# Kernel tuning notes

Measured on AMD Instinct MI355X. Metric: run time of the kernel, lower is better.

The kernel has to match this reference:

```python
import jax, jax.numpy as jnp
import numpy as np

N_NODES = 100000
N_EDGES = 1600000
N_GRAPHS = 512
IN_CH = 64
HID = 64
OUT_CH = 2
NC = 3


def setup_inputs() -> dict:
    key = jax.random.key(0)
    ks = jax.random.split(key, 10)
    x = jax.random.normal(ks[0], (N_NODES, IN_CH), dtype=jnp.float32)
    edge_index = jax.random.randint(ks[1], (2, N_EDGES), 0, N_NODES, dtype=jnp.int64)
    batch = jnp.sort(jax.random.randint(ks[2], (N_NODES,), 0, N_GRAPHS, dtype=jnp.int64))
    s = 1.0 / np.sqrt(HID)
    W_rel = jax.random.normal(ks[3], (NC, HID, HID), dtype=jnp.float32) * s
    W_root = jax.random.normal(ks[4], (NC, HID, HID), dtype=jnp.float32) * s
    b_conv = jax.random.normal(ks[5], (NC, HID), dtype=jnp.float32) * s
    W1 = jax.random.normal(ks[6], (HID, 2 * HID), dtype=jnp.float32) * s
    b1 = jax.random.normal(ks[7], (2 * HID,), dtype=jnp.float32) * s
    W2 = jax.random.normal(ks[8], (2 * HID, OUT_CH), dtype=jnp.float32) * (1.0 / np.sqrt(2 * HID))
    b2 = jax.random.normal(ks[9], (OUT_CH,), dtype=jnp.float32) * (1.0 / np.sqrt(2 * HID))
    return {"x": x, "edge_index": edge_index, "batch": batch,
            "W_rel": W_rel, "W_root": W_root, "b_conv": b_conv,
            "W1": W1, "b1": b1, "W2": W2, "b2": b2}


def reference(x, edge_index, batch, W_rel, W_root, b_conv, W1, b1, W2, b2):
    src, dst = edge_index[0], edge_index[1]
    h = x
    for i in range(NC):
        # PyG GraphConv(aggr='add'): lin_rel(scatter_add(h[src] -> dst)) + lin_root(h)
        agg = jax.ops.segment_sum(h[src], dst, num_segments=N_NODES)  # [N, HID]
        h = jax.nn.relu(agg @ W_rel[i] + b_conv[i] + h @ W_root[i])
    pooled = jax.ops.segment_sum(h, batch, num_segments=N_GRAPHS)  # [G, HID]
    # MLP readout [HID, 2*HID, OUT]
    out = jax.nn.sigmoid(jax.nn.relu(pooled @ W1 + b1) @ W2 + b2)  # [G, OUT]
    return out, pooled
```

## Files before the change

### kernel.cpp

```cpp
#include <hip/hip_runtime.h>
#include <math.h>

#define N_NODES 100000
#define N_EDGES 1600000
#define N_GRAPHS 512
#define HID 64
#define NC 3

#define NBUCK 782
#define EPB 8192
#define NPBLK 196
#define PSTRIDE 3072
#define BSTRIDE 4096
#define DUMMY N_NODES
#define SRCMASK 0x1FFFF

typedef unsigned int uint;

__device__ __forceinline__ ushort f2bf(float f) {
    uint u = __float_as_uint(f);
    u += 0x7fffu + ((u >> 16) & 1u);
    return (ushort)(u >> 16);
}
__device__ __forceinline__ uint packbf2(float a, float b) {
    return (uint)f2bf(a) | ((uint)f2bf(b) << 16);
}


__global__ __launch_bounds__(512) void partition_kernel(const int* __restrict__ src,
                                                        const int* __restrict__ dst,
                                                        int* __restrict__ ccursor,
                                                        uint* __restrict__ part) {
    __shared__ int cnt[NBUCK];
    __shared__ int base[NBUCK];
    __shared__ int cur[NBUCK];
    for (int i = threadIdx.x; i < NBUCK; i += 512) { cnt[i] = 0; cur[i] = 0; }
    __syncthreads();
    const int4* d4 = (const int4*)dst;
    const int4* s4 = (const int4*)src;
    int i0 = blockIdx.x * (EPB / 4);
    int i1 = min(i0 + EPB / 4, N_EDGES / 4);
    for (int i = i0 + threadIdx.x; i < i1; i += 512) {
        int4 d = d4[i];
        atomicAdd(&cnt[d.x >> 7], 1);
        atomicAdd(&cnt[d.y >> 7], 1);
        atomicAdd(&cnt[d.z >> 7], 1);
        atomicAdd(&cnt[d.w >> 7], 1);
    }
    __syncthreads();
    for (int i = threadIdx.x; i < NBUCK; i += 512)
        base[i] = cnt[i] ? (i * PSTRIDE + atomicAdd(&ccursor[i], cnt[i])) : 0;
    __syncthreads();
    for (int i = i0 + threadIdx.x; i < i1; i += 512) {
        int4 d = d4[i];
        int4 s = s4[i];
        int b0 = d.x >> 7; part[base[b0] + atomicAdd(&cur[b0], 1)] = ((uint)(d.x & 127) << 17) | (uint)s.x;
        int b1 = d.y >> 7; part[base[b1] + atomicAdd(&cur[b1], 1)] = ((uint)(d.y & 127) << 17) | (uint)s.y;
        int b2 = d.z >> 7; part[base[b2] + atomicAdd(&cur[b2], 1)] = ((uint)(d.z & 127) << 17) | (uint)s.z;
        int b3 = d.w >> 7; part[base[b3] + atomicAdd(&cur[b3], 1)] = ((uint)(d.w & 127) << 17) | (uint)s.w;
    }
}


__global__ __launch_bounds__(256) void bcsr_kernel(const uint* __restrict__ part,
                                                   const int* __restrict__ ccursor,
                                                   int* __restrict__ row_ptr,
                                                   int* __restrict__ pdeg,
                                                   int* __restrict__ col) {
    __shared__ int deg[128];
    __shared__ int cur[128];
    __shared__ int pre[128];
    __shared__ int ss[256];
    int b = blockIdx.x;
    int t = threadIdx.x;
    int s0 = b * PSTRIDE;
    int s1 = s0 + ccursor[b];
    if (t < 128) { deg[t] = 0; cur[t] = 0; }
    __syncthreads();
    for (int e = s0 + t; e < s1; e += 256)
        atomicAdd(&deg[part[e] >> 17], 1);
    __syncthreads();
    int v = (t < 128) ? ((deg[t] + 7) & ~7) : 0;
    int val = v;
    ss[t] = val;
    __syncthreads();
    for (int off = 1; off < 256; off <<= 1) {
        int o = (t >= off) ? ss[t - off] : 0;
        __syncthreads();
        val += o;
        ss[t] = val;
        __syncthreads();
    }
    if (t < 128) pre[t] = val - v;
    __syncthreads();
    int base = b * BSTRIDE;
    int node = b * 128 + t;
    if (t < 128 && node < N_NODES) {
        row_ptr[node] = base + pre[t];
        pdeg[node] = v;
    }
    for (int e = s0 + t; e < s1; e += 256) {
        uint p = part[e];
        int nl = p >> 17;
        int r = atomicAdd(&cur[nl], 1);
        col[base + pre[nl] + r] = (int)(p & SRCMASK);
    }
    __syncthreads();
    if (t < 128) {
        for (int i = deg[t]; i < v; i++)
            col[base + pre[t] + i] = DUMMY;
    }
}


__global__ __launch_bounds__(256) void cvt_kernel(const float* __restrict__ x,
                                                  ushort* __restrict__ hX,
                                                  ushort* __restrict__ hA,
                                                  ushort* __restrict__ hB) {
    if (blockIdx.x == 0 && threadIdx.x < HID) {
        hX[(size_t)N_NODES * HID + threadIdx.x] = 0;
        hA[(size_t)N_NODES * HID + threadIdx.x] = 0;
        hB[(size_t)N_NODES * HID + threadIdx.x] = 0;
    }
    int i = blockIdx.x * blockDim.x + threadIdx.x;
    int stride = gridDim.x * blockDim.x;
    const float4* x4 = (const float4*)x;
    for (; i < N_NODES * HID / 4; i += stride) {
        float4 v = x4[i];
        uint2 o;
        o.x = packbf2(v.x, v.y);
        o.y = packbf2(v.z, v.w);
        *(uint2*)(hX + (size_t)i * 4) = o;
    }
}


__global__ __launch_bounds__(256) void wprep_kernel(const float* __restrict__ W_rel,
                                                    const float* __restrict__ W_root,
                                                    ushort* __restrict__ WT) {
    int i = blockIdx.x * blockDim.x + threadIdx.x;
    if (i >= NC * 2 * HID * HID) return;
    int l = i / (2 * HID * HID);
    int rem = i % (2 * HID * HID);
    int m = rem / (HID * HID);
    int j = rem % (HID * HID);
    int colc = j / HID;
    int k = j % HID;
    const float* W = (m ? W_root : W_rel) + l * HID * HID;
    WT[i] = f2bf(W[k * HID + colc]);
}


#define ACC4(A, v) { A.x += __uint_as_float((v).x << 16); \
                     A.y += __uint_as_float((v).x & 0xffff0000u); \
                     A.z += __uint_as_float((v).y << 16); \
                     A.w += __uint_as_float((v).y & 0xffff0000u); }

__global__ __launch_bounds__(256) void gather_kernel(
    const ushort* __restrict__ hin, ushort* __restrict__ agg,
    const int* __restrict__ row_ptr, const int* __restrict__ pdeg,
    const int* __restrict__ col)
{
    int lane = threadIdx.x & 63;
    int slot = lane >> 4;
    int ch   = (lane & 15) * 4;
    int gwid = (blockIdx.x * blockDim.x + threadIdx.x) >> 6;
    int nwaves = (gridDim.x * blockDim.x) >> 6;

    for (int n0 = gwid * 4; n0 < N_NODES; n0 += nwaves * 4) {
        int n = n0 + slot;
        const int* row = col + row_ptr[n];
        int pd = pdeg[n];
        float4 a0 = {0.f,0.f,0.f,0.f}, a1 = {0.f,0.f,0.f,0.f};
        float4 a2 = {0.f,0.f,0.f,0.f}, a3 = {0.f,0.f,0.f,0.f};
        for (int e = 0; e < pd; e += 8) {
            int4 ca = *(const int4*)(row + e);
            int4 cb = *(const int4*)(row + e + 4);
            uint2 v0 = *(const uint2*)(hin + (size_t)ca.x * HID + ch);
            uint2 v1 = *(const uint2*)(hin + (size_t)ca.y * HID + ch);
            uint2 v2 = *(const uint2*)(hin + (size_t)ca.z * HID + ch);
            uint2 v3 = *(const uint2*)(hin + (size_t)ca.w * HID + ch);
            uint2 v4 = *(const uint2*)(hin + (size_t)cb.x * HID + ch);
            uint2 v5 = *(const uint2*)(hin + (size_t)cb.y * HID + ch);
            uint2 v6 = *(const uint2*)(hin + (size_t)cb.z * HID + ch);
            uint2 v7 = *(const uint2*)(hin + (size_t)cb.w * HID + ch);
            ACC4(a0, v0); ACC4(a1, v1); ACC4(a2, v2); ACC4(a3, v3);
            ACC4(a0, v4); ACC4(a1, v5); ACC4(a2, v6); ACC4(a3, v7);
        }
        a0.x += a1.x + a2.x + a3.x;
        a0.y += a1.y + a2.y + a3.y;
        a0.z += a1.z + a2.z + a3.z;
        a0.w += a1.w + a2.w + a3.w;
        uint2 o;
        o.x = packbf2(a0.x, a0.y);
        o.y = packbf2(a0.z, a0.w);
        *(uint2*)(agg + (size_t)n * HID + ch) = o;
    }
}


__global__ __launch_bounds__(256) void transform_kernel(
    const ushort* __restrict__ hin, const ushort* __restrict__ agg,
    ushort* __restrict__ hout, const ushort* __restrict__ WTl,
    const float* __restrict__ bias)
{
    typedef __attribute__((ext_vector_type(8))) short short8;
    typedef __attribute__((ext_vector_type(4))) float f32x4;
    __shared__ float lds[4][16][68];
    int lane = threadIdx.x & 63;
    int wid  = threadIdx.x >> 6;
    int mrow = lane & 15;
    int kg   = lane >> 4;
    int gw = (blockIdx.x * blockDim.x + threadIdx.x) >> 6;
    int nw = (gridDim.x * blockDim.x) >> 6;

    short8 Bf[4][4];
#pragma unroll
    for (int c = 0; c < 4; c++)
#pragma unroll
        for (int m = 0; m < 2; m++)
#pragma unroll
            for (int h = 0; h < 2; h++)
                Bf[c][m * 2 + h] = *(const short8*)(
                    WTl + m * HID * HID + (c * 16 + mrow) * HID + h * 32 + kg * 8);

    float bv[4];
#pragma unroll
    for (int c = 0; c < 4; c++) bv[c] = bias[c * 16 + mrow];

    for (int ng = gw; ng < N_NODES / 16; ng += nw) {
        size_t rb = ((size_t)ng * 16 + mrow) * HID + kg * 8;
        short8 Ah0 = *(const short8*)(hin + rb);
        short8 Ah1 = *(const short8*)(hin + rb + 32);
        short8 Aa0 = *(const short8*)(agg + rb);
        short8 Aa1 = *(const short8*)(agg + rb + 32);
#pragma unroll
        for (int c = 0; c < 4; c++) {
            f32x4 acc = {0.f, 0.f, 0.f, 0.f};
            acc = __builtin_amdgcn_mfma_f32_16x16x32_bf16(Aa0, Bf[c][0], acc, 0, 0, 0);
            acc = __builtin_amdgcn_mfma_f32_16x16x32_bf16(Aa1, Bf[c][1], acc, 0, 0, 0);
            acc = __builtin_amdgcn_mfma_f32_16x16x32_bf16(Ah0, Bf[c][2], acc, 0, 0, 0);
            acc = __builtin_amdgcn_mfma_f32_16x16x32_bf16(Ah1, Bf[c][3], acc, 0, 0, 0);
#pragma unroll
            for (int r = 0; r < 4; r++)
                lds[wid][kg * 4 + r][c * 16 + mrow] = fmaxf(acc[r] + bv[c], 0.f);
        }
        asm volatile("s_waitcnt lgkmcnt(0)" ::: "memory");
        const float* lr = &lds[wid][mrow][kg * 16];
        float4 f0 = *(const float4*)(lr + 0);
        float4 f1 = *(const float4*)(lr + 4);
        float4 f2 = *(const float4*)(lr + 8);
        float4 f3 = *(const float4*)(lr + 12);
        uint4 o0, o1;
        o0.x = packbf2(f0.x, f0.y); o0.y = packbf2(f0.z, f0.w);
        o0.z = packbf2(f1.x, f1.y); o0.w = packbf2(f1.z, f1.w);
        o1.x = packbf2(f2.x, f2.y); o1.y = packbf2(f2.z, f2.w);
        o1.z = packbf2(f3.x, f3.y); o1.w = packbf2(f3.z, f3.w);
        ushort* orow = hout + ((size_t)ng * 16 + mrow) * HID + kg * 16;
        *(uint4*)(orow) = o0;
        *(uint4*)(orow + 8) = o1;
    }
}


__global__ __launch_bounds__(256) void pool_kernel(
    const ushort* __restrict__ h, const int* __restrict__ batch,
    float* __restrict__ pooled_ws) {
    const int CH = 64;
    int lane = threadIdx.x & 63;
    int gwid = (blockIdx.x * blockDim.x + threadIdx.x) >> 6;
    int n0 = gwid * CH;
    if (n0 >= N_NODES) return;
    int nend = min(n0 + CH, N_NODES);
    int cur = batch[n0];
    float acc = 0.f;
    for (int n = n0; n < nend; n++) {
        int g = batch[n];
        if (g != cur) {
            atomicAdd(&pooled_ws[cur * HID + lane], acc);
            acc = 0.f;
            cur = g;
        }
        acc += __uint_as_float(((uint)h[(size_t)n * HID + lane]) << 16);
    }
    atomicAdd(&pooled_ws[cur * HID + lane], acc);
}


__global__ void mlp_kernel(const float* __restrict__ pooled_ws,
                           const float* __restrict__ W1, const float* __restrict__ b1,
                           const float* __restrict__ W2, const float* __restrict__ b2,
                           float* __restrict__ out, float* __restrict__ pooled_out) {
    __shared__ float sp[HID];
    __shared__ float red[4];
    int g = blockIdx.x, t = threadIdx.x;
    if (t < HID) {
        float v = pooled_ws[g * HID + t];
        sp[t] = v;
        pooled_out[g * HID + t] = v;
    }
    __syncthreads();
    float acc = b1[t];
#pragma unroll
    for (int k = 0; k < HID; k++) acc = fmaf(sp[k], W1[k * 128 + t], acc);
    float hid = fmaxf(acc, 0.f);
    float p0 = hid * W2[t * 2 + 0];
    float p1 = hid * W2[t * 2 + 1];
    for (int off = 32; off > 0; off >>= 1) {
        p0 += __shfl_down(p0, off, 64);
        p1 += __shfl_down(p1, off, 64);
    }
    int wave = t >> 6, lane = t & 63;
    if (lane == 0) { red[wave * 2 + 0] = p0; red[wave * 2 + 1] = p1; }
    __syncthreads();
    if (t == 0) {
        float o0 = red[0] + red[2] + b2[0];
        float o1 = red[1] + red[3] + b2[1];
        out[g * 2 + 0] = 1.f / (1.f + expf(-o0));
        out[g * 2 + 1] = 1.f / (1.f + expf(-o1));
    }
}


extern "C" void kernel_launch(void* const* d_in, const int* in_sizes, int n_in,
                              void* d_out, int out_size, void* d_ws, size_t ws_size,
                              hipStream_t stream) {
    const float* x      = (const float*)d_in[0];
    const int*   ei     = (const int*)d_in[1];
    const int*   batch  = (const int*)d_in[2];
    const float* W_rel  = (const float*)d_in[3];
    const float* W_root = (const float*)d_in[4];
    const float* b_conv = (const float*)d_in[5];
    const float* W1     = (const float*)d_in[6];
    const float* b1     = (const float*)d_in[7];
    const float* W2     = (const float*)d_in[8];
    const float* b2     = (const float*)d_in[9];

    float* outp       = (float*)d_out;
    float* pooled_out = (float*)d_out + N_GRAPHS * 2;

    const size_t HROWS_B = ((size_t)(N_NODES + 1) * HID * 2 + 255) & ~(size_t)255;

    char* ws = (char*)d_ws;
    size_t off = 0;
    ushort* hX = (ushort*)(ws + off); off += HROWS_B;
    ushort* hA = (ushort*)(ws + off); off += HROWS_B;
    ushort* hB = (ushort*)(ws + off); off += HROWS_B;
    ushort* gg = (ushort*)(ws + off); off += ((size_t)N_NODES * HID * 2 + 255) & ~(size_t)255;
    ushort* WT = (ushort*)(ws + off); off += ((size_t)NC * 2 * HID * HID * 2 + 255) & ~(size_t)255;
    uint* part    = (uint*)(ws + off); off += (size_t)NBUCK * PSTRIDE * 4;
    int* colidx   = (int*)(ws + off); off += (size_t)NBUCK * BSTRIDE * 4;
    int* row_ptr  = (int*)(ws + off); off += (size_t)(N_NODES + 4) * 4;
    int* pdeg     = (int*)(ws + off); off += (size_t)(N_NODES + 4) * 4;
    int* ccursor  = (int*)(ws + off); off += (size_t)NBUCK * 4;
    float* pooled_ws = (float*)(ws + off); off += (size_t)N_GRAPHS * HID * 4;

    const int* esrc = ei;
    const int* edst = ei + N_EDGES;

    hipMemsetAsync(ccursor, 0, (size_t)NBUCK * 4, stream);
    hipMemsetAsync(pooled_ws, 0, (size_t)N_GRAPHS * HID * 4, stream);

    cvt_kernel<<<2048, 256, 0, stream>>>(x, hX, hA, hB);
    wprep_kernel<<<(NC * 2 * HID * HID + 255) / 256, 256, 0, stream>>>(W_rel, W_root, WT);

    partition_kernel<<<NPBLK, 512, 0, stream>>>(esrc, edst, ccursor, part);
    bcsr_kernel<<<NBUCK, 256, 0, stream>>>(part, ccursor, row_ptr, pdeg, colidx);

    gather_kernel<<<2048, 256, 0, stream>>>(hX, gg, row_ptr, pdeg, colidx);
    transform_kernel<<<512, 256, 0, stream>>>(hX, gg, hA, WT + 0 * 2 * HID * HID, b_conv + 0 * HID);
    gather_kernel<<<2048, 256, 0, stream>>>(hA, gg, row_ptr, pdeg, colidx);
    transform_kernel<<<512, 256, 0, stream>>>(hA, gg, hB, WT + 1 * 2 * HID * HID, b_conv + 1 * HID);
    gather_kernel<<<2048, 256, 0, stream>>>(hB, gg, row_ptr, pdeg, colidx);
    transform_kernel<<<512, 256, 0, stream>>>(hB, gg, hA, WT + 2 * 2 * HID * HID, b_conv + 2 * HID);

    pool_kernel<<<391, 256, 0, stream>>>(hA, batch, pooled_ws);
    mlp_kernel<<<N_GRAPHS, 128, 0, stream>>>(pooled_ws, W1, b1, W2, b2, outp, pooled_out);
}
```

Baseline: 290.5 us.

## Fuse gather and transform into one per-layer kernel via LDS staging

Merges the neighbour gather and the MFMA transform of each GraphConv layer into one layer_kernel. Each wave aggregates 16 nodes into LDS and feeds them straight to the bf16 MFMA, so the global agg buffer's write and re-read go away and three launches are saved. It also folds weight prep into the conversion kernel and doubles the partition block size and edges per block. The cost is a fixed one-block-per-64-nodes grid with no grid-stride loop, and padding rows/row_ptr past N_NODES so the last partial tile reads valid zeros.

```diff
diff --git a/kernel.cpp b/kernel.cpp
--- a/kernel.cpp
+++ b/kernel.cpp
@@ -8,12 +8,13 @@
 #define NC 3
 
 #define NBUCK 782
-#define EPB 8192
-#define NPBLK 196
+#define EPB 16384
+#define NPBLK 98
 #define PSTRIDE 3072
 #define BSTRIDE 4096
 #define DUMMY N_NODES
 #define SRCMASK 0x1FFFF
+#define NFBLK 1563
 
 typedef unsigned int uint;
 
@@ -27,20 +28,20 @@
 }
 
 
-__global__ __launch_bounds__(512) void partition_kernel(const int* __restrict__ src,
-                                                        const int* __restrict__ dst,
-                                                        int* __restrict__ ccursor,
-                                                        uint* __restrict__ part) {
+__global__ __launch_bounds__(1024) void partition_kernel(const int* __restrict__ src,
+                                                         const int* __restrict__ dst,
+                                                         int* __restrict__ ccursor,
+                                                         uint* __restrict__ part) {
     __shared__ int cnt[NBUCK];
     __shared__ int base[NBUCK];
     __shared__ int cur[NBUCK];
-    for (int i = threadIdx.x; i < NBUCK; i += 512) { cnt[i] = 0; cur[i] = 0; }
+    for (int i = threadIdx.x; i < NBUCK; i += 1024) { cnt[i] = 0; cur[i] = 0; }
     __syncthreads();
     const int4* d4 = (const int4*)dst;
     const int4* s4 = (const int4*)src;
     int i0 = blockIdx.x * (EPB / 4);
     int i1 = min(i0 + EPB / 4, N_EDGES / 4);
-    for (int i = i0 + threadIdx.x; i < i1; i += 512) {
+    for (int i = i0 + threadIdx.x; i < i1; i += 1024) {
         int4 d = d4[i];
         atomicAdd(&cnt[d.x >> 7], 1);
         atomicAdd(&cnt[d.y >> 7], 1);
@@ -48,10 +49,10 @@
         atomicAdd(&cnt[d.w >> 7], 1);
     }
     __syncthreads();
-    for (int i = threadIdx.x; i < NBUCK; i += 512)
+    for (int i = threadIdx.x; i < NBUCK; i += 1024)
         base[i] = cnt[i] ? (i * PSTRIDE + atomicAdd(&ccursor[i], cnt[i])) : 0;
     __syncthreads();
-    for (int i = i0 + threadIdx.x; i < i1; i += 512) {
+    for (int i = i0 + threadIdx.x; i < i1; i += 1024) {
         int4 d = d4[i];
         int4 s = s4[i];
         int b0 = d.x >> 7; part[base[b0] + atomicAdd(&cur[b0], 1)] = ((uint)(d.x & 127) << 17) | (uint)s.x;
@@ -116,38 +117,41 @@
 __global__ __launch_bounds__(256) void cvt_kernel(const float* __restrict__ x,
                                                   ushort* __restrict__ hX,
                                                   ushort* __restrict__ hA,
-                                                  ushort* __restrict__ hB) {
-    if (blockIdx.x == 0 && threadIdx.x < HID) {
-        hX[(size_t)N_NODES * HID + threadIdx.x] = 0;
-        hA[(size_t)N_NODES * HID + threadIdx.x] = 0;
-        hB[(size_t)N_NODES * HID + threadIdx.x] = 0;
-    }
-    int i = blockIdx.x * blockDim.x + threadIdx.x;
+                                                  ushort* __restrict__ hB,
+                                                  const float* __restrict__ W_rel,
+                                                  const float* __restrict__ W_root,
+                                                  ushort* __restrict__ WT,
+                                                  int* __restrict__ row_ptr,
+                                                  int* __restrict__ pdeg) {
+    int gid = blockIdx.x * blockDim.x + threadIdx.x;
     int stride = gridDim.x * blockDim.x;
+    if (gid < HID) {
+        hX[(size_t)N_NODES * HID + gid] = 0;
+        hA[(size_t)N_NODES * HID + gid] = 0;
+        hB[(size_t)N_NODES * HID + gid] = 0;
+    }
+    if (gid < 64) {
+        pdeg[N_NODES + gid] = 0;
+        row_ptr[N_NODES + gid] = 0;
+    }
     const float4* x4 = (const float4*)x;
-    for (; i < N_NODES * HID / 4; i += stride) {
+    for (int i = gid; i < N_NODES * HID / 4; i += stride) {
         float4 v = x4[i];
         uint2 o;
         o.x = packbf2(v.x, v.y);
         o.y = packbf2(v.z, v.w);
         *(uint2*)(hX + (size_t)i * 4) = o;
     }
-}
-
-
-__global__ __launch_bounds__(256) void wprep_kernel(const float* __restrict__ W_rel,
-                                                    const float* __restrict__ W_root,
-                                                    ushort* __restrict__ WT) {
-    int i = blockIdx.x * blockDim.x + threadIdx.x;
-    if (i >= NC * 2 * HID * HID) return;
-    int l = i / (2 * HID * HID);
-    int rem = i % (2 * HID * HID);
-    int m = rem / (HID * HID);
-    int j = rem % (HID * HID);
-    int colc = j / HID;
-    int k = j % HID;
-    const float* W = (m ? W_root : W_rel) + l * HID * HID;
-    WT[i] = f2bf(W[k * HID + colc]);
+    for (int i = gid; i < NC * 2 * HID * HID; i += stride) {
+        int l = i / (2 * HID * HID);
+        int rem = i % (2 * HID * HID);
+        int m = rem / (HID * HID);
+        int j = rem % (HID * HID);
+        int colc = j / HID;
+        int k = j % HID;
+        const float* W = (m ? W_root : W_rel) + l * HID * HID;
+        WT[i] = f2bf(W[k * HID + colc]);
+    }
 }
 
 
@@ -156,19 +160,25 @@
                      A.z += __uint_as_float((v).y << 16); \
                      A.w += __uint_as_float((v).y & 0xffff0000u); }
 
-__global__ __launch_bounds__(256) void gather_kernel(
-    const ushort* __restrict__ hin, ushort* __restrict__ agg,
+__global__ __launch_bounds__(256) void layer_kernel(
+    const ushort* __restrict__ hin, ushort* __restrict__ hout,
     const int* __restrict__ row_ptr, const int* __restrict__ pdeg,
-    const int* __restrict__ col)
+    const int* __restrict__ col, const ushort* __restrict__ WTl,
+    const float* __restrict__ bias)
 {
+    typedef __attribute__((ext_vector_type(8))) short short8;
+    typedef __attribute__((ext_vector_type(4))) float f32x4;
+    __shared__ ushort sagg[4][16][80];
     int lane = threadIdx.x & 63;
+    int w = threadIdx.x >> 6;
+    int nbase = blockIdx.x * 64 + w * 16;
+
     int slot = lane >> 4;
-    int ch   = (lane & 15) * 4;
-    int gwid = (blockIdx.x * blockDim.x + threadIdx.x) >> 6;
-    int nwaves = (gridDim.x * blockDim.x) >> 6;
-
-    for (int n0 = gwid * 4; n0 < N_NODES; n0 += nwaves * 4) {
-        int n = n0 + slot;
+    int ch = (lane & 15) * 4;
+#pragma unroll
+    for (int p = 0; p < 4; p++) {
+        int nl = p * 4 + slot;
+        int n = nbase + nl;
         const int* row = col + row_ptr[n];
         int pd = pdeg[n];
         float4 a0 = {0.f,0.f,0.f,0.f}, a1 = {0.f,0.f,0.f,0.f};
@@ -194,26 +204,11 @@
         uint2 o;
         o.x = packbf2(a0.x, a0.y);
         o.y = packbf2(a0.z, a0.w);
-        *(uint2*)(agg + (size_t)n * HID + ch) = o;
-    }
-}
-
-
-__global__ __launch_bounds__(256) void transform_kernel(
-    const ushort* __restrict__ hin, const ushort* __restrict__ agg,
-    ushort* __restrict__ hout, const ushort* __restrict__ WTl,
-    const float* __restrict__ bias)
-{
-    typedef __attribute__((ext_vector_type(8))) short short8;
-    typedef __attribute__((ext_vector_type(4))) float f32x4;
-    __shared__ float lds[4][16][68];
-    int lane = threadIdx.x & 63;
-    int wid  = threadIdx.x >> 6;
+        *(uint2*)&sagg[w][nl][ch] = o;
+    }
+
     int mrow = lane & 15;
-    int kg   = lane >> 4;
-    int gw = (blockIdx.x * blockDim.x + threadIdx.x) >> 6;
-    int nw = (gridDim.x * blockDim.x) >> 6;
-
+    int kg = lane >> 4;
     short8 Bf[4][4];
 #pragma unroll
     for (int c = 0; c < 4; c++)
@@ -223,40 +218,33 @@
             for (int h = 0; h < 2; h++)
                 Bf[c][m * 2 + h] = *(const short8*)(
                     WTl + m * HID * HID + (c * 16 + mrow) * HID + h * 32 + kg * 8);
-
     float bv[4];
 #pragma unroll
     for (int c = 0; c < 4; c++) bv[c] = bias[c * 16 + mrow];
 
-    for (int ng = gw; ng < N_NODES / 16; ng += nw) {
-        size_t rb = ((size_t)ng * 16 + mrow) * HID + kg * 8;
-        short8 Ah0 = *(const short8*)(hin + rb);
-        short8 Ah1 = *(const short8*)(hin + rb + 32);
-        short8 Aa0 = *(const short8*)(agg + rb);
-        short8 Aa1 = *(const short8*)(agg + rb + 32);
-#pragma unroll
-        for (int c = 0; c < 4; c++) {
-            f32x4 acc = {0.f, 0.f, 0.f, 0.f};
-            acc = __builtin_amdgcn_mfma_f32_16x16x32_bf16(Aa0, Bf[c][0], acc, 0, 0, 0);
-            acc = __builtin_amdgcn_mfma_f32_16x16x32_bf16(Aa1, Bf[c][1], acc, 0, 0, 0);
-            acc = __builtin_amdgcn_mfma_f32_16x16x32_bf16(Ah0, Bf[c][2], acc, 0, 0, 0);
-            acc = __builtin_amdgcn_mfma_f32_16x16x32_bf16(Ah1, Bf[c][3], acc, 0, 0, 0);
-#pragma unroll
-            for (int r = 0; r < 4; r++)
-                lds[wid][kg * 4 + r][c * 16 + mrow] = fmaxf(acc[r] + bv[c], 0.f);
-        }
-        asm volatile("s_waitcnt lgkmcnt(0)" ::: "memory");
-        const float* lr = &lds[wid][mrow][kg * 16];
-        float4 f0 = *(const float4*)(lr + 0);
-        float4 f1 = *(const float4*)(lr + 4);
-        float4 f2 = *(const float4*)(lr + 8);
-        float4 f3 = *(const float4*)(lr + 12);
-        uint4 o0, o1;
-        o0.x = packbf2(f0.x, f0.y); o0.y = packbf2(f0.z, f0.w);
-        o0.z = packbf2(f1.x, f1.y); o0.w = packbf2(f1.z, f1.w);
-        o1.x = packbf2(f2.x, f2.y); o1.y = packbf2(f2.z, f2.w);
-        o1.z = packbf2(f3.x, f3.y); o1.w = packbf2(f3.z, f3.w);
-        ushort* orow = hout + ((size_t)ng * 16 + mrow) * HID + kg * 16;
+    int n = nbase + mrow;
+    size_t rb = (size_t)n * HID + kg * 8;
+    short8 Ah0 = *(const short8*)(hin + rb);
+    short8 Ah1 = *(const short8*)(hin + rb + 32);
+    short8 Aa0 = *(const short8*)&sagg[w][mrow][kg * 8];
+    short8 Aa1 = *(const short8*)&sagg[w][mrow][32 + kg * 8];
+
+#pragma unroll
+    for (int c = 0; c < 4; c++) {
+        f32x4 acc = {0.f, 0.f, 0.f, 0.f};
+        acc = __builtin_amdgcn_mfma_f32_16x16x32_bf16(Aa0, Bf[c][0], acc, 0, 0, 0);
+        acc = __builtin_amdgcn_mfma_f32_16x16x32_bf16(Aa1, Bf[c][1], acc, 0, 0, 0);
+        acc = __builtin_amdgcn_mfma_f32_16x16x32_bf16(Ah0, Bf[c][2], acc, 0, 0, 0);
+        acc = __builtin_amdgcn_mfma_f32_16x16x32_bf16(Ah1, Bf[c][3], acc, 0, 0, 0);
+#pragma unroll
+        for (int r = 0; r < 4; r++)
+            sagg[w][kg * 4 + r][c * 16 + mrow] = f2bf(fmaxf(acc[r] + bv[c], 0.f));
+    }
+
+    if (n < N_NODES) {
+        uint4 o0 = *(const uint4*)&sagg[w][mrow][kg * 16];
+        uint4 o1 = *(const uint4*)&sagg[w][mrow][kg * 16 + 8];
+        ushort* orow = hout + (size_t)n * HID + kg * 16;
         *(uint4*)(orow) = o0;
         *(uint4*)(orow + 8) = o1;
     }
@@ -339,19 +327,18 @@
     float* outp       = (float*)d_out;
     float* pooled_out = (float*)d_out + N_GRAPHS * 2;
 
-    const size_t HROWS_B = ((size_t)(N_NODES + 1) * HID * 2 + 255) & ~(size_t)255;
+    const size_t HROWS_B = ((size_t)(N_NODES + 64) * HID * 2 + 255) & ~(size_t)255;
 
     char* ws = (char*)d_ws;
     size_t off = 0;
     ushort* hX = (ushort*)(ws + off); off += HROWS_B;
     ushort* hA = (ushort*)(ws + off); off += HROWS_B;
     ushort* hB = (ushort*)(ws + off); off += HROWS_B;
-    ushort* gg = (ushort*)(ws + off); off += ((size_t)N_NODES * HID * 2 + 255) & ~(size_t)255;
     ushort* WT = (ushort*)(ws + off); off += ((size_t)NC * 2 * HID * HID * 2 + 255) & ~(size_t)255;
     uint* part    = (uint*)(ws + off); off += (size_t)NBUCK * PSTRIDE * 4;
     int* colidx   = (int*)(ws + off); off += (size_t)NBUCK * BSTRIDE * 4;
-    int* row_ptr  = (int*)(ws + off); off += (size_t)(N_NODES + 4) * 4;
-    int* pdeg     = (int*)(ws + off); off += (size_t)(N_NODES + 4) * 4;
+    int* row_ptr  = (int*)(ws + off); off += (size_t)(N_NODES + 68) * 4;
+    int* pdeg     = (int*)(ws + off); off += (size_t)(N_NODES + 68) * 4;
     int* ccursor  = (int*)(ws + off); off += (size_t)NBUCK * 4;
     float* pooled_ws = (float*)(ws + off); off += (size_t)N_GRAPHS * HID * 4;
 
@@ -361,18 +348,17 @@
     hipMemsetAsync(ccursor, 0, (size_t)NBUCK * 4, stream);
     hipMemsetAsync(pooled_ws, 0, (size_t)N_GRAPHS * HID * 4, stream);
 
-    cvt_kernel<<<2048, 256, 0, stream>>>(x, hX, hA, hB);
-    wprep_kernel<<<(NC * 2 * HID * HID + 255) / 256, 256, 0, stream>>>(W_rel, W_root, WT);
-
-    partition_kernel<<<NPBLK, 512, 0, stream>>>(esrc, edst, ccursor, part);
+    cvt_kernel<<<2048, 256, 0, stream>>>(x, hX, hA, hB, W_rel, W_root, WT, row_ptr, pdeg);
+
+    partition_kernel<<<NPBLK, 1024, 0, stream>>>(esrc, edst, ccursor, part);
     bcsr_kernel<<<NBUCK, 256, 0, stream>>>(part, ccursor, row_ptr, pdeg, colidx);
 
-    gather_kernel<<<2048, 256, 0, stream>>>(hX, gg, row_ptr, pdeg, colidx);
-    transform_kernel<<<512, 256, 0, stream>>>(hX, gg, hA, WT + 0 * 2 * HID * HID, b_conv + 0 * HID);
-    gather_kernel<<<2048, 256, 0, stream>>>(hA, gg, row_ptr, pdeg, colidx);
-    transform_kernel<<<512, 256, 0, stream>>>(hA, gg, hB, WT + 1 * 2 * HID * HID, b_conv + 1 * HID);
-    gather_kernel<<<2048, 256, 0, stream>>>(hB, gg, row_ptr, pdeg, colidx);
-    transform_kernel<<<512, 256, 0, stream>>>(hB, gg, hA, WT + 2 * 2 * HID * HID, b_conv + 2 * HID);
+    layer_kernel<<<NFBLK, 256, 0, stream>>>(hX, hA, row_ptr, pdeg, colidx,
+                                            WT + 0 * 2 * HID * HID, b_conv + 0 * HID);
+    layer_kernel<<<NFBLK, 256, 0, stream>>>(hA, hB, row_ptr, pdeg, colidx,
+                                            WT + 1 * 2 * HID * HID, b_conv + 1 * HID);
+    layer_kernel<<<NFBLK, 256, 0, stream>>>(hB, hA, row_ptr, pdeg, colidx,
+                                            WT + 2 * 2 * HID * HID, b_conv + 2 * HID);
 
     pool_kernel<<<391, 256, 0, stream>>>(hA, batch, pooled_ws);
     mlp_kernel<<<N_GRAPHS, 128, 0, stream>>>(pooled_ws, W1, b1, W2, b2, outp, pooled_out);
```

New measurement: 315.2 us. +8.5%, slower.
